# Kernel optimization log

Measured on AMD Instinct MI355X. Metric: run time of the kernel, lower is better.

The kernel has to match this reference:

```python
import jax, jax.numpy as jnp
import numpy as np

B, C, T, V = 32, 64, 128, 25
OUT, REL, TS = 64, 8, 9  # out_channels, rel_channels=in//8, time_step


def setup_inputs() -> dict:
    key = jax.random.key(0)
    ks = jax.random.split(key, 6)
    s = lambda fan: 1.0 / np.sqrt(fan)
    return {
        "x": jax.random.normal(ks[0], (B, C, T, V), jnp.float32),
        "A": jax.random.normal(ks[1], (V, V), jnp.float32) * 0.1,
        "w1": jax.random.normal(ks[2], (REL, C), jnp.float32) * s(C),
        "b1": jnp.zeros((REL,), jnp.float32),
        "w2": jax.random.normal(ks[3], (REL, C), jnp.float32) * s(C),
        "b2": jnp.zeros((REL,), jnp.float32),
        "w3": jax.random.normal(ks[4], (OUT, C), jnp.float32) * s(C),
        "b3": jnp.zeros((OUT,), jnp.float32),
        "w4": jax.random.normal(ks[5], (C * TS, REL), jnp.float32) * s(REL),
        "b4": jnp.zeros((C * TS,), jnp.float32),
    }


def reference(x, A, w1, b1, w2, b2, w3, b3, w4, b4):
    alpha = 1.0
    # conv1/conv2 are 1x1 convs followed by mean over T (bias survives the mean)
    x1 = jnp.einsum('rc,bctv->brv', w1, x) / T + b1[None, :, None]   # (B,R,V)
    x2 = jnp.einsum('rc,bctv->brv', w2, x) / T + b2[None, :, None]   # (B,R,V)
    d = jnp.tanh(x1[:, :, :, None] - x2[:, :, None, :])              # (B,R,V,V)
    # conv4 (1x1): rel -> C*TS, then *alpha + A broadcast
    adj = jnp.einsum('or,bruv->bouv', w4, d) + b4[None, :, None, None]
    adj = adj * alpha + A[None, None]                                 # (B,C*TS,V,V)
    # reshape (B,C,TS,V1,V2) -> (B,C,V1=j(in),V2=i(out),TS); dim-2 index i selects output vertex
    W = adj.reshape(B, C, TS, V, V).transpose(0, 1, 3, 4, 2)          # (B,C,Vj,Vi,TS)
    # causal left-pad on T, then sliding windows of length TS (stride=1)
    xp = jnp.pad(x, ((0, 0), (0, 0), (TS - 1, 0), (0, 0)))            # (B,C,T+TS-1,V)
    xw = jnp.stack([xp[:, :, k:k + T, :] for k in range(TS)], axis=-1)  # (B,C,T,V,TS)
    # grouped dynamic conv: z[b,c,t,i] = sum_{j,k} xw[b,c,t,j,k] * W[b,c,j,i,k]
    z = jnp.einsum('bctjk,bcjik->bcti', xw, W)                        # (B,C,T,V)
    # conv3 (1x1): C -> OUT
    out = jnp.einsum('oc,bctv->botv', w3, z) + b3[None, :, None, None]
    return out
```

## Files before the change

kernel.cpp:

```cpp
#include <hip/hip_runtime.h>
#include <math.h>

#define Bc 32
#define Cc 64
#define Tc 128
#define Vc 25
#define OUTC 64
#define RELC 8
#define TSC 9

typedef __bf16 bf16x8 __attribute__((ext_vector_type(8)));
typedef float f32x4 __attribute__((ext_vector_type(4)));

static __device__ __forceinline__ ushort f2bf(float f) {
    union { float f; uint u; } v; v.f = f;
    uint u = v.u;
    u += 0x7fff + ((u >> 16) & 1);
    return (ushort)(u >> 16);
}

static __device__ __forceinline__ bf16x8 ldfrag(const ushort* row, int dwoff) {
    const uint* p = (const uint*)row + dwoff;
    uint4 u;
    u.x = p[0]; u.y = p[1]; u.z = p[2]; u.w = p[3];
    return __builtin_bit_cast(bf16x8, u);
}

__global__ __launch_bounds__(256) void k_mean(const float* __restrict__ x,
                                              float* __restrict__ xm) {
    int bc = blockIdx.x;
    int v  = threadIdx.x & 31;
    int tg = threadIdx.x >> 5;
    const float* xp = x + (size_t)bc * Tc * Vc;
    float s = 0.f;
    if (v < Vc) {
        for (int t = tg; t < Tc; t += 8) s += xp[t * Vc + v];
    }
    __shared__ float red[8][32];
    red[tg][v] = s;
    __syncthreads();
    if (tg == 0 && v < Vc) {
        float tot = 0.f;
#pragma unroll
        for (int g = 0; g < 8; ++g) tot += red[g][v];
        xm[bc * Vc + v] = tot * (1.0f / Tc);
    }
}

__global__ __launch_bounds__(256) void k_rel(const float* __restrict__ xm,
                                             const float* __restrict__ w1,
                                             const float* __restrict__ b1,
                                             const float* __restrict__ w2,
                                             const float* __restrict__ b2,
                                             float* __restrict__ d) {
    int b = blockIdx.x;
    __shared__ float sxm[Cc * Vc];
    __shared__ float sx1[RELC * Vc];
    __shared__ float sx2[RELC * Vc];
    int tid = threadIdx.x;
    for (int idx = tid; idx < Cc * Vc; idx += 256)
        sxm[idx] = xm[(size_t)b * Cc * Vc + idx];
    __syncthreads();
    for (int idx = tid; idx < 2 * RELC * Vc; idx += 256) {
        int which = idx / (RELC * Vc);
        int rv = idx % (RELC * Vc);
        int r = rv / Vc, v = rv % Vc;
        const float* w = which ? w2 : w1;
        float acc = which ? b2[r] : b1[r];
        for (int c = 0; c < Cc; ++c) acc += w[r * Cc + c] * sxm[c * Vc + v];
        (which ? sx2 : sx1)[rv] = acc;
    }
    __syncthreads();
    float* dp = d + (size_t)b * RELC * Vc * Vc;
    for (int idx = tid; idx < RELC * Vc * Vc; idx += 256) {
        int r  = idx / (Vc * Vc);
        int jj = (idx / Vc) % Vc;
        int ii = idx % Vc;
        dp[idx] = tanhf(sx1[r * Vc + jj] - sx2[r * Vc + ii]);
    }
}

#define XSROW 38
#define XSROWS 136
__global__ __launch_bounds__(256, 4) void k_dynconv(const float* __restrict__ x,
                                                    const float* __restrict__ d,
                                                    const float* __restrict__ w4,
                                                    const float* __restrict__ b4,
                                                    const float* __restrict__ A,
                                                    ushort* __restrict__ z) {
    int bc = blockIdx.x;
    int b = bc / Cc, c = bc % Cc;
    __shared__ ushort xs[XSROWS * XSROW];
    __shared__ ushort sB[TSC * 32 * XSROW];
    __shared__ float sw4[TSC * RELC];
    __shared__ float sb4[TSC];
    int tid = threadIdx.x;

    uint* sBu = (uint*)sB;
    for (int idx = tid; idx < TSC * 32 * (XSROW / 2); idx += 256) sBu[idx] = 0;
    const float* xp = x + (size_t)bc * Tc * Vc;
    uint* xsu = (uint*)xs;
    for (int idx = tid; idx < XSROWS * (XSROW / 2); idx += 256) {
        int row = idx / (XSROW / 2), pr = idx % (XSROW / 2);
        int j0 = pr * 2;
        float f0 = 0.f, f1 = 0.f;
        if (row >= TSC - 1) {
            const float* xr = xp + (row - (TSC - 1)) * Vc;
            if (j0 < Vc) f0 = xr[j0];
            if (j0 + 1 < Vc) f1 = xr[j0 + 1];
        }
        xsu[idx] = (uint)f2bf(f0) | ((uint)f2bf(f1) << 16);
    }
    if (tid < TSC * RELC) sw4[tid] = w4[(c * TSC + tid / RELC) * RELC + tid % RELC];
    if (tid < TSC) sb4[tid] = b4[c * TSC + tid];
    __syncthreads();

    const float* dp = d + (size_t)b * RELC * Vc * Vc;
    for (int p = tid; p < Vc * Vc; p += 256) {
        int j = p / Vc, i = p % Vc;
        float dv[RELC];
#pragma unroll
        for (int r = 0; r < RELC; ++r) dv[r] = dp[r * Vc * Vc + p];
        float av = A[p];
#pragma unroll
        for (int k = 0; k < TSC; ++k) {
            float acc = sb4[k] + av;
#pragma unroll
            for (int r = 0; r < RELC; ++r) acc += sw4[k * RELC + r] * dv[r];
            sB[(k * 32 + i) * XSROW + j] = f2bf(acc);
        }
    }
    __syncthreads();

    int wv = tid >> 6, lane = tid & 63, lr = lane & 15, q = lane >> 4;
    f32x4 acc[2][2];
#pragma unroll
    for (int mi = 0; mi < 2; ++mi)
#pragma unroll
        for (int ni = 0; ni < 2; ++ni) acc[mi][ni] = (f32x4)0.0f;

    for (int k = 0; k < TSC; ++k) {
        int r0 = (wv * 2) * 16 + lr + k;
        bf16x8 a0 = ldfrag(xs + r0 * XSROW, q * 4);
        bf16x8 a1 = ldfrag(xs + (r0 + 16) * XSROW, q * 4);
        bf16x8 bb0 = ldfrag(sB + (k * 32 + lr) * XSROW, q * 4);
        bf16x8 bb1 = ldfrag(sB + (k * 32 + 16 + lr) * XSROW, q * 4);
        acc[0][0] = __builtin_amdgcn_mfma_f32_16x16x32_bf16(a0, bb0, acc[0][0], 0, 0, 0);
        acc[0][1] = __builtin_amdgcn_mfma_f32_16x16x32_bf16(a0, bb1, acc[0][1], 0, 0, 0);
        acc[1][0] = __builtin_amdgcn_mfma_f32_16x16x32_bf16(a1, bb0, acc[1][0], 0, 0, 0);
        acc[1][1] = __builtin_amdgcn_mfma_f32_16x16x32_bf16(a1, bb1, acc[1][1], 0, 0, 0);
    }

    ushort* zp = z + (size_t)bc * Tc * Vc;
#pragma unroll
    for (int mi = 0; mi < 2; ++mi) {
        int t0 = (wv * 2 + mi) * 16 + q * 4;
#pragma unroll
        for (int ni = 0; ni < 2; ++ni) {
            int i = ni * 16 + lr;
            if (i < Vc) {
#pragma unroll
                for (int r = 0; r < 4; ++r)
                    zp[(t0 + r) * Vc + i] = f2bf(acc[mi][ni][r]);
            }
        }
    }
}

#define SZROW 70
#define COLT 256
__global__ __launch_bounds__(256, 2) void k_conv3(const ushort* __restrict__ z,
                                                  const float* __restrict__ w3,
                                                  const float* __restrict__ b3,
                                                  float* __restrict__ out) {
    int b = blockIdx.y;
    int col0 = blockIdx.x * COLT;
    __shared__ ushort sz[COLT * SZROW];
    __shared__ ushort sw3[OUTC * SZROW];
    int tid = threadIdx.x;

    for (int idx = tid; idx < OUTC * Cc; idx += 256)
        sw3[(idx >> 6) * SZROW + (idx & 63)] = f2bf(w3[idx]);

    const ushort* zb = z + (size_t)b * Cc * Tc * Vc;
#pragma unroll
    for (int rep = 0; rep < 8; ++rep) {
        int it = rep * 256 + tid;
        int cc = it >> 5, ch = it & 31;
        int col = ch * 8, gcol = col0 + col;
        ushort vals[8];
        if (gcol < Tc * Vc) {
            const uint4* src = (const uint4*)(zb + (size_t)cc * Tc * Vc + gcol);
            uint4 u = *src;
            uint ua[4] = {u.x, u.y, u.z, u.w};
#pragma unroll
            for (int e = 0; e < 8; ++e) vals[e] = (ushort)(ua[e >> 1] >> ((e & 1) * 16));
        } else {
#pragma unroll
            for (int e = 0; e < 8; ++e) vals[e] = 0;
        }
#pragma unroll
        for (int e = 0; e < 8; ++e) sz[(col + e) * SZROW + cc] = vals[e];
    }
    __syncthreads();

    int wv = tid >> 6, lane = tid & 63, lr = lane & 15, q = lane >> 4;
    f32x4 acc[4][4];
#pragma unroll
    for (int mi = 0; mi < 4; ++mi)
#pragma unroll
        for (int ni = 0; ni < 4; ++ni) acc[mi][ni] = (f32x4)0.0f;

#pragma unroll
    for (int ks = 0; ks < 2; ++ks) {
        bf16x8 a[4], bb[4];
#pragma unroll
        for (int mi = 0; mi < 4; ++mi)
            a[mi] = ldfrag(sz + ((wv * 4 + mi) * 16 + lr) * SZROW, ks * 16 + q * 4);
#pragma unroll
        for (int ni = 0; ni < 4; ++ni)
            bb[ni] = ldfrag(sw3 + (ni * 16 + lr) * SZROW, ks * 16 + q * 4);
#pragma unroll
        for (int mi = 0; mi < 4; ++mi)
#pragma unroll
            for (int ni = 0; ni < 4; ++ni)
                acc[mi][ni] = __builtin_amdgcn_mfma_f32_16x16x32_bf16(a[mi], bb[ni], acc[mi][ni], 0, 0, 0);
    }

#pragma unroll
    for (int ni = 0; ni < 4; ++ni) {
        int o = ni * 16 + lr;
        float bias = b3[o];
        float* ob = out + ((size_t)b * OUTC + o) * Tc * Vc;
#pragma unroll
        for (int mi = 0; mi < 4; ++mi) {
            int cb = col0 + (wv * 4 + mi) * 16 + q * 4;
            if (cb < Tc * Vc) {
                float4 st = {acc[mi][ni][0] + bias, acc[mi][ni][1] + bias,
                             acc[mi][ni][2] + bias, acc[mi][ni][3] + bias};
                *(float4*)(ob + cb) = st;
            }
        }
    }
}

extern "C" void kernel_launch(void* const* d_in, const int* in_sizes, int n_in,
                              void* d_out, int out_size, void* d_ws, size_t ws_size,
                              hipStream_t stream) {
    const float* x  = (const float*)d_in[0];
    const float* A  = (const float*)d_in[1];
    const float* w1 = (const float*)d_in[2];
    const float* b1 = (const float*)d_in[3];
    const float* w2 = (const float*)d_in[4];
    const float* b2 = (const float*)d_in[5];
    const float* w3 = (const float*)d_in[6];
    const float* b3 = (const float*)d_in[7];
    const float* w4 = (const float*)d_in[8];
    const float* b4 = (const float*)d_in[9];
    float* out = (float*)d_out;

    float* ws = (float*)d_ws;
    float* xm = ws;
    float* dd = ws + (size_t)Bc * Cc * Vc;
    ushort* zz = (ushort*)(ws + 211200);

    k_mean<<<Bc * Cc, 256, 0, stream>>>(x, xm);
    k_rel<<<Bc, 256, 0, stream>>>(xm, w1, b1, w2, b2, dd);
    k_dynconv<<<Bc * Cc, 256, 0, stream>>>(x, dd, w4, b4, A, zz);
    k_conv3<<<dim3((Tc * Vc + COLT - 1) / COLT, Bc), 256, 0, stream>>>(zz, w3, b3, out);
}
```

Measured before the change: 134.2 us.

## Store relation tanh in bf16 transposed layout, split k_rel, shrink conv3 tiles

k_rel now runs one block per (batch, rel) pair and writes tanh differences as bf16 in a [v,v,rel] layout. k_dynconv can then load all eight relation values per vertex pair with a single 16-byte read instead of eight strided float loads. The goal is less traffic for the d tensor, which k_dynconv re-reads from all 64 channel blocks per batch, and more parallelism in k_rel. k_conv3 uses 128-column tiles with higher occupancy and drops its bounds checks, since T*V divides evenly. The dynconv k-loop is also fully unrolled, and the bf16 storage of d adds some rounding error.

```diff
diff --git a/kernel.cpp b/kernel.cpp
--- a/kernel.cpp
+++ b/kernel.cpp
@@ -17,6 +17,11 @@
     uint u = v.u;
     u += 0x7fff + ((u >> 16) & 1);
     return (ushort)(u >> 16);
+}
+
+static __device__ __forceinline__ float bf2f(uint bits) {
+    union { uint u; float f; } v; v.u = bits << 16;
+    return v.f;
 }
 
 static __device__ __forceinline__ bf16x8 ldfrag(const ushort* row, int dwoff) {
@@ -52,38 +57,33 @@
                                              const float* __restrict__ b1,
                                              const float* __restrict__ w2,
                                              const float* __restrict__ b2,
-                                             float* __restrict__ d) {
-    int b = blockIdx.x;
+                                             ushort* __restrict__ dT) {
+    int b = blockIdx.x >> 3, r = blockIdx.x & 7;
     __shared__ float sxm[Cc * Vc];
-    __shared__ float sx1[RELC * Vc];
-    __shared__ float sx2[RELC * Vc];
+    __shared__ float s1[Vc], s2[Vc];
     int tid = threadIdx.x;
     for (int idx = tid; idx < Cc * Vc; idx += 256)
         sxm[idx] = xm[(size_t)b * Cc * Vc + idx];
     __syncthreads();
-    for (int idx = tid; idx < 2 * RELC * Vc; idx += 256) {
-        int which = idx / (RELC * Vc);
-        int rv = idx % (RELC * Vc);
-        int r = rv / Vc, v = rv % Vc;
+    if (tid < 2 * Vc) {
+        int which = tid / Vc, v = tid % Vc;
         const float* w = which ? w2 : w1;
         float acc = which ? b2[r] : b1[r];
         for (int c = 0; c < Cc; ++c) acc += w[r * Cc + c] * sxm[c * Vc + v];
-        (which ? sx2 : sx1)[rv] = acc;
-    }
-    __syncthreads();
-    float* dp = d + (size_t)b * RELC * Vc * Vc;
-    for (int idx = tid; idx < RELC * Vc * Vc; idx += 256) {
-        int r  = idx / (Vc * Vc);
-        int jj = (idx / Vc) % Vc;
-        int ii = idx % Vc;
-        dp[idx] = tanhf(sx1[r * Vc + jj] - sx2[r * Vc + ii]);
+        (which ? s2 : s1)[v] = acc;
+    }
+    __syncthreads();
+    ushort* dp = dT + (size_t)b * Vc * Vc * RELC + r;
+    for (int p = tid; p < Vc * Vc; p += 256) {
+        int j = p / Vc, i = p % Vc;
+        dp[p * RELC] = f2bf(tanhf(s1[j] - s2[i]));
     }
 }
 
 #define XSROW 38
 #define XSROWS 136
 __global__ __launch_bounds__(256, 4) void k_dynconv(const float* __restrict__ x,
-                                                    const float* __restrict__ d,
+                                                    const ushort* __restrict__ dT,
                                                     const float* __restrict__ w4,
                                                     const float* __restrict__ b4,
                                                     const float* __restrict__ A,
@@ -115,12 +115,15 @@
     if (tid < TSC) sb4[tid] = b4[c * TSC + tid];
     __syncthreads();
 
-    const float* dp = d + (size_t)b * RELC * Vc * Vc;
+    const ushort* dp = dT + (size_t)b * Vc * Vc * RELC;
     for (int p = tid; p < Vc * Vc; p += 256) {
         int j = p / Vc, i = p % Vc;
+        uint4 u = *(const uint4*)(dp + p * RELC);
+        uint ua[4] = {u.x, u.y, u.z, u.w};
         float dv[RELC];
 #pragma unroll
-        for (int r = 0; r < RELC; ++r) dv[r] = dp[r * Vc * Vc + p];
+        for (int e = 0; e < RELC; ++e)
+            dv[e] = bf2f((ua[e >> 1] >> ((e & 1) * 16)) & 0xffffu);
         float av = A[p];
 #pragma unroll
         for (int k = 0; k < TSC; ++k) {
@@ -139,6 +142,7 @@
 #pragma unroll
         for (int ni = 0; ni < 2; ++ni) acc[mi][ni] = (f32x4)0.0f;
 
+#pragma unroll
     for (int k = 0; k < TSC; ++k) {
         int r0 = (wv * 2) * 16 + lr + k;
         bf16x8 a0 = ldfrag(xs + r0 * XSROW, q * 4);
@@ -168,8 +172,8 @@
 }
 
 #define SZROW 70
-#define COLT 256
-__global__ __launch_bounds__(256, 2) void k_conv3(const ushort* __restrict__ z,
+#define COLT 128
+__global__ __launch_bounds__(256, 5) void k_conv3(const ushort* __restrict__ z,
                                                   const float* __restrict__ w3,
                                                   const float* __restrict__ b3,
                                                   float* __restrict__ out) {
@@ -184,44 +188,37 @@
 
     const ushort* zb = z + (size_t)b * Cc * Tc * Vc;
 #pragma unroll
-    for (int rep = 0; rep < 8; ++rep) {
+    for (int rep = 0; rep < 4; ++rep) {
         int it = rep * 256 + tid;
-        int cc = it >> 5, ch = it & 31;
-        int col = ch * 8, gcol = col0 + col;
-        ushort vals[8];
-        if (gcol < Tc * Vc) {
-            const uint4* src = (const uint4*)(zb + (size_t)cc * Tc * Vc + gcol);
-            uint4 u = *src;
-            uint ua[4] = {u.x, u.y, u.z, u.w};
-#pragma unroll
-            for (int e = 0; e < 8; ++e) vals[e] = (ushort)(ua[e >> 1] >> ((e & 1) * 16));
-        } else {
-#pragma unroll
-            for (int e = 0; e < 8; ++e) vals[e] = 0;
-        }
-#pragma unroll
-        for (int e = 0; e < 8; ++e) sz[(col + e) * SZROW + cc] = vals[e];
+        int cc = it >> 4, ch = it & 15;
+        int col = ch * 8;
+        const uint4* src = (const uint4*)(zb + (size_t)cc * Tc * Vc + col0 + col);
+        uint4 u = *src;
+        uint ua[4] = {u.x, u.y, u.z, u.w};
+#pragma unroll
+        for (int e = 0; e < 8; ++e)
+            sz[(col + e) * SZROW + cc] = (ushort)(ua[e >> 1] >> ((e & 1) * 16));
     }
     __syncthreads();
 
     int wv = tid >> 6, lane = tid & 63, lr = lane & 15, q = lane >> 4;
-    f32x4 acc[4][4];
-#pragma unroll
-    for (int mi = 0; mi < 4; ++mi)
+    f32x4 acc[2][4];
+#pragma unroll
+    for (int mi = 0; mi < 2; ++mi)
 #pragma unroll
         for (int ni = 0; ni < 4; ++ni) acc[mi][ni] = (f32x4)0.0f;
 
 #pragma unroll
     for (int ks = 0; ks < 2; ++ks) {
-        bf16x8 a[4], bb[4];
-#pragma unroll
-        for (int mi = 0; mi < 4; ++mi)
-            a[mi] = ldfrag(sz + ((wv * 4 + mi) * 16 + lr) * SZROW, ks * 16 + q * 4);
+        bf16x8 a[2], bb[4];
+#pragma unroll
+        for (int mi = 0; mi < 2; ++mi)
+            a[mi] = ldfrag(sz + ((wv * 2 + mi) * 16 + lr) * SZROW, ks * 16 + q * 4);
 #pragma unroll
         for (int ni = 0; ni < 4; ++ni)
             bb[ni] = ldfrag(sw3 + (ni * 16 + lr) * SZROW, ks * 16 + q * 4);
 #pragma unroll
-        for (int mi = 0; mi < 4; ++mi)
+        for (int mi = 0; mi < 2; ++mi)
 #pragma unroll
             for (int ni = 0; ni < 4; ++ni)
                 acc[mi][ni] = __builtin_amdgcn_mfma_f32_16x16x32_bf16(a[mi], bb[ni], acc[mi][ni], 0, 0, 0);
@@ -233,13 +230,11 @@
         float bias = b3[o];
         float* ob = out + ((size_t)b * OUTC + o) * Tc * Vc;
 #pragma unroll
-        for (int mi = 0; mi < 4; ++mi) {
-            int cb = col0 + (wv * 4 + mi) * 16 + q * 4;
-            if (cb < Tc * Vc) {
-                float4 st = {acc[mi][ni][0] + bias, acc[mi][ni][1] + bias,
-                             acc[mi][ni][2] + bias, acc[mi][ni][3] + bias};
-                *(float4*)(ob + cb) = st;
-            }
+        for (int mi = 0; mi < 2; ++mi) {
+            int cb = col0 + (wv * 2 + mi) * 16 + q * 4;
+            float4 st = {acc[mi][ni][0] + bias, acc[mi][ni][1] + bias,
+                         acc[mi][ni][2] + bias, acc[mi][ni][3] + bias};
+            *(float4*)(ob + cb) = st;
         }
     }
 }
@@ -261,11 +256,11 @@
 
     float* ws = (float*)d_ws;
     float* xm = ws;
-    float* dd = ws + (size_t)Bc * Cc * Vc;
-    ushort* zz = (ushort*)(ws + 211200);
+    ushort* dT = (ushort*)(ws + 51200);
+    ushort* zz = (ushort*)(ws + 51200 + 80000);
 
     k_mean<<<Bc * Cc, 256, 0, stream>>>(x, xm);
-    k_rel<<<Bc, 256, 0, stream>>>(xm, w1, b1, w2, b2, dd);
-    k_dynconv<<<Bc * Cc, 256, 0, stream>>>(x, dd, w4, b4, A, zz);
-    k_conv3<<<dim3((Tc * Vc + COLT - 1) / COLT, Bc), 256, 0, stream>>>(zz, w3, b3, out);
-}
+    k_rel<<<Bc * RELC, 256, 0, stream>>>(xm, w1, b1, w2, b2, dT);
+    k_dynconv<<<Bc * Cc, 256, 0, stream>>>(x, dT, w4, b4, A, zz);
+    k_conv3<<<dim3((Tc * Vc) / COLT, Bc), 256, 0, stream>>>(zz, w3, b3, out);
+}
```

New measurement: 131.7 us. No clear change (-1.9%).
